# Kernel optimization log

Hardware: AMD Instinct MI355X
Metric: run time of the kernel (lower is better)

Reference implementation:

```python
import jax, jax.numpy as jnp
import numpy as np

O, D, E, K, H, A = 1024, 1024, 16, 4, 2048, 64  # option_dim, obs_dim, num_experts, k, moe_hidden, act_dim
LOSS_COEF = 0.01


def cv_squared(x):
    # torch .var() is unbiased (ddof=1)
    eps = 1e-10
    return jnp.var(x, ddof=1) / (jnp.mean(x) ** 2 + eps)


def setup_inputs() -> dict:
    key = jax.random.key(0)
    ks = jax.random.split(key, 8)
    s = 0.02
    return {
        "obs": jax.random.normal(ks[0], (O, D), jnp.float32),
        # original inits w_gate to zeros (degenerate top-k); use small random for a meaningful baseline
        "w_gate": jax.random.normal(ks[1], (O, D, E), jnp.float32) * s,
        "w1": jax.random.normal(ks[2], (E, D, H), jnp.float32) * s,   # expert MLP layer 1
        "b1": jnp.zeros((E, H), jnp.float32),
        "w2": jax.random.normal(ks[3], (E, H, A), jnp.float32) * s,   # expert MLP layer 2
        "b2": jnp.zeros((E, A), jnp.float32),
        "last_w": jax.random.normal(ks[4], (O, D, A), jnp.float32),   # last_w_layer
        "last_b": jax.random.normal(ks[5], (O, A), jnp.float32),      # last_b_layer
    }


def reference(obs, w_gate, w1, b1, w2, b2, last_w, last_b):
    # ---- noisy_top_k_gating (this version applies no noise) ----
    logits = jnp.einsum('od,ode->oe', obs, w_gate)                    # [O, E]
    top_vals, top_idx = jax.lax.top_k(logits, K + 1)
    topk_gates = jax.nn.softmax(top_vals[:, :K], axis=1)              # softmax over top-k logits
    rows = jnp.arange(O)[:, None]
    gates = jnp.zeros_like(logits).at[rows, top_idx[:, :K]].set(topk_gates)  # scatter -> [O, E]
    importance = gates.sum(axis=1)
    load = (gates > 0).sum(axis=1).astype(jnp.float32)                # faithful to original (sum over dim 1)
    loss = (cv_squared(importance) + cv_squared(load)) * LOSS_COEF
    # ---- dispatch / expert MLPs / combine (dense-over-experts equivalent; zero gates kill non-top-k) ----
    h = jax.nn.relu(jnp.einsum('od,edh->oeh', obs, w1) + b1[None])    # [O, E, H]
    y = jnp.einsum('oe,oeh,eha->oa', gates, h, w2) + gates @ b2       # [O, A]
    # ---- action head ----
    mu = jnp.einsum('od,oda->oa', obs, last_w) + last_b               # [O, A]
    action_probs = jax.nn.softmax(mu, axis=-1)
    z = (action_probs == 0.0).astype(action_probs.dtype) * 1e-08
    log_action_probs = jnp.log(action_probs + z)
    return (action_probs, log_action_probs, y, loss)
```

## Files before the change

### kernel.cpp

```cpp
#include <hip/hip_runtime.h>
#include <hip/hip_bf16.h>
#include <math.h>

#define O_ 1024
#define D_ 1024
#define E_ 16
#define K_ 4
#define H_ 2048
#define A_ 64
#define LOSS_COEF 0.01f

#define FLT_MIN_NORMAL 1.17549435e-38f

using floatx4 = __attribute__((ext_vector_type(4))) float;
using fragb   = __attribute__((ext_vector_type(8))) short;

static __device__ __forceinline__ ushort f2bf(float f) {
    unsigned u = __builtin_bit_cast(unsigned, f);
    u += 0x7fffu + ((u >> 16) & 1u);
    return (ushort)(u >> 16);
}

static __device__ __forceinline__ void gld_lds16(const void* g, void* l) {
    __builtin_amdgcn_global_load_lds(
        (const __attribute__((address_space(1))) void*)g,
        (__attribute__((address_space(3))) void*)l, 16, 0, 0);
}

__global__ __launch_bounds__(256) void front_kernel(
    const float* __restrict__ obs, const float* __restrict__ w_gate,
    const float* __restrict__ b2,
    const float* __restrict__ w1, const float* __restrict__ w2,
    int* __restrict__ cnt, int* __restrict__ rows, float* __restrict__ gatev,
    float* __restrict__ imp, float* __restrict__ loadv,
    ushort* __restrict__ obs_bf, float* __restrict__ yout,
    ushort* __restrict__ w1T, ushort* __restrict__ w2T)
{
    const int bid = blockIdx.x;
    const int t = threadIdx.x;
    __shared__ __align__(16) char sh[9344];

    if (bid < 1024) {
        const int o = bid;
        float* xs            = (float*)sh;
        float (*part)[20]    = (float(*)[20])(sh + 4096);
        float* logits        = (float*)(sh + 9216);
        int*   sidx          = (int*)(sh + 9280);
        float* sgate         = (float*)(sh + 9296);

        const float4* xrow = (const float4*)(obs + (size_t)o * D_);
        for (int i = t; i < D_ / 4; i += 256) ((float4*)xs)[i] = xrow[i];
        __syncthreads();

        const int dg = t >> 2, e4 = t & 3;
        const float4* wg = (const float4*)(w_gate + (size_t)o * (D_ * E_));
        float4 acc = make_float4(0.f, 0.f, 0.f, 0.f);
        #pragma unroll 4
        for (int i = 0; i < 16; ++i) {
            int d = dg + (i << 6);
            float4 w = wg[d * 4 + e4];
            float x = xs[d];
            acc.x += x * w.x; acc.y += x * w.y; acc.z += x * w.z; acc.w += x * w.w;
        }
        *(float4*)&part[dg][e4 * 4] = acc;
        __syncthreads();
        if (t < E_) {
            float s = 0.f;
            for (int g = 0; g < 64; ++g) s += part[g][t];
            logits[t] = s;
        }
        __syncthreads();
        if (t == 0) {
            float lv[E_];
            #pragma unroll
            for (int i = 0; i < E_; ++i) lv[i] = logits[i];
            int idx[K_]; float val[K_];
            bool used[E_] = {};
            for (int k = 0; k < K_; ++k) {
                int bi = 0; float bv = -INFINITY;
                for (int i = 0; i < E_; ++i)
                    if (!used[i] && lv[i] > bv) { bv = lv[i]; bi = i; }
                used[bi] = true; idx[k] = bi; val[k] = bv;
            }
            float m = val[0];
            float ex[K_]; float s = 0.f;
            for (int k = 0; k < K_; ++k) { ex[k] = expf(val[k] - m); s += ex[k]; }
            float inv = 1.f / s;
            float sumg = 0.f; int ld = 0;
            for (int k = 0; k < K_; ++k) {
                float g = ex[k] * inv;
                sidx[k] = idx[k]; sgate[k] = g;
                int pos = atomicAdd(&cnt[idx[k]], 1);
                rows[idx[k] * O_ + pos]  = o;
                gatev[idx[k] * O_ + pos] = g;
                sumg += g;
                if (g > 0.f) ld++;
            }
            imp[o] = sumg;
            loadv[o] = (float)ld;
        }

        {
            float4 v = ((const float4*)xs)[t];
            ushort4 u;
            u.x = f2bf(v.x); u.y = f2bf(v.y); u.z = f2bf(v.z); u.w = f2bf(v.w);
            ((ushort4*)(obs_bf + (size_t)o * D_))[t] = u;
        }
        __syncthreads();

        if (t < A_) {
            float accy = 0.f;
            #pragma unroll
            for (int k = 0; k < K_; ++k)
                accy += sgate[k] * b2[sidx[k] * A_ + t];
            yout[(size_t)o * A_ + t] = accy;
        }
        return;
    }

    {
        int id = bid - 1024;
        const float* src; ushort* dst; int R, C, c0, r0, e;
        if (id < 8192) {
            c0 = (id & 31) * 64; r0 = ((id >> 5) & 15) * 64; e = id >> 9;
            src = w1; dst = w1T; R = D_; C = H_;
        } else {
            id -= 8192;
            c0 = 0; r0 = (id & 31) * 64; e = id >> 5;
            src = w2; dst = w2T; R = H_; C = A_;
        }

        ushort (*tile)[72] = (ushort(*)[72])sh;
        const float* s = src + (size_t)e * R * C;
        const int rr = t >> 4, cq = t & 15;
        #pragma unroll
        for (int i = 0; i < 4; ++i) {
            int r = rr + i * 16;
            float4 v = *(const float4*)(s + (size_t)(r0 + r) * C + c0 + cq * 4);
            ushort4 u;
            u.x = f2bf(v.x); u.y = f2bf(v.y); u.z = f2bf(v.z); u.w = f2bf(v.w);
            *(ushort4*)&tile[r][cq * 4] = u;
        }
        __syncthreads();
        ushort* dbase = dst + (size_t)e * R * C;
        const int cc = t >> 4, rq = t & 15;
        #pragma unroll
        for (int i = 0; i < 4; ++i) {
            int c = cc + i * 16;
            ushort4 u;
            u.x = tile[rq * 4 + 0][c];
            u.y = tile[rq * 4 + 1][c];
            u.z = tile[rq * 4 + 2][c];
            u.w = tile[rq * 4 + 3][c];
            *(ushort4*)(dbase + (size_t)(c0 + c) * R + r0 + rq * 4) = u;
        }
    }
}

__global__ __launch_bounds__(256, 4) void mega_kernel(
    const ushort* __restrict__ obs_bf, const ushort* __restrict__ w1T,
    const float* __restrict__ b1, const ushort* __restrict__ w2T,
    const int* __restrict__ cnt, const int* __restrict__ rows,
    const float* __restrict__ gatev, float* __restrict__ y,
    const float* __restrict__ obs, const float* __restrict__ last_w,
    const float* __restrict__ last_b,
    float* __restrict__ probs, float* __restrict__ logprobs,
    const float* __restrict__ imp, const float* __restrict__ loadv,
    float* __restrict__ out_loss)
{
    const int bid = blockIdx.x;
    const int t = threadIdx.x;

    __shared__ __align__(16) ushort smem[17408];
    __shared__ int   rid_s[128];
    __shared__ float rgate_s[128];
    __shared__ float b1s[128];
    __shared__ float mean1, mean2;

    if (bid == 0) {
        float* ls1 = (float*)smem;
        float* ls2 = ls1 + 256;
        float a[4], b[4];
        float pa = 0.f, pb = 0.f;
        #pragma unroll
        for (int j = 0; j < 4; ++j) {
            a[j] = imp[t + 256 * j]; b[j] = loadv[t + 256 * j];
            pa += a[j]; pb += b[j];
        }
        ls1[t] = pa; ls2[t] = pb; __syncthreads();
        for (int s = 128; s > 0; s >>= 1) {
            if (t < s) { ls1[t] += ls1[t + s]; ls2[t] += ls2[t + s]; }
            __syncthreads();
        }
        if (t == 0) { mean1 = ls1[0] / O_; mean2 = ls2[0] / O_; }
        __syncthreads();
        pa = 0.f; pb = 0.f;
        #pragma unroll
        for (int j = 0; j < 4; ++j) {
            float d1 = a[j] - mean1, d2 = b[j] - mean2;
            pa += d1 * d1; pb += d2 * d2;
        }
        ls1[t] = pa; ls2[t] = pb; __syncthreads();
        for (int s = 128; s > 0; s >>= 1) {
            if (t < s) { ls1[t] += ls1[t + s]; ls2[t] += ls2[t + s]; }
            __syncthreads();
        }
        if (t == 0) {
            float var1 = ls1[0] / (O_ - 1), var2 = ls2[0] / (O_ - 1);
            const float eps = 1e-10f;
            out_loss[0] = (var1 / (mean1 * mean1 + eps) + var2 / (mean2 * mean2 + eps)) * LOSS_COEF;
        }
        return;
    }

    if (bid <= 2048) {
        const int id  = bid - 1;
        const int xcd = id & 7;
        const int r8  = (id >> 3) & 7;
        const int phi = id >> 6;
        const int p   = (phi << 3) | xcd;
        const int e   = p >> 4, ht = p & 15, rt = r8;
        const int n = cnt[e];
        if (rt * 128 >= n) return;

        const int wv = t >> 6, l = t & 63;
        const int lm = l & 15, q = l >> 4;
        const int wr = wv >> 1, wc = wv & 1;

        if (t < 128) {
            int gi = rt * 128 + t;
            rid_s[t]   = (gi < n) ? rows[e * O_ + gi]  : -1;
            rgate_s[t] = (gi < n) ? gatev[e * O_ + gi] : 0.f;
        } else {
            b1s[t - 128] = b1[e * H_ + ht * 128 + (t - 128)];
        }
        __syncthreads();

        const int swe = ((l & 7) ^ (l >> 3)) << 3;
        const ushort* asrc[4];
        const ushort* bsrc[4];
        #pragma unroll
        for (int j = 0; j < 4; ++j) {
            int r = (j * 4 + wv) * 8 + (l >> 3);
            int arow = rid_s[r]; if (arow < 0) arow = 0;
            asrc[j] = obs_bf + (size_t)arow * D_ + swe;
            bsrc[j] = w1T + ((size_t)(e * H_ + ht * 128 + r)) * D_ + swe;
        }

        auto stage = [&](int kc) {
            ushort* ab_ = &smem[0];
            ushort* bb_ = &smem[8192];
            const int ko = kc * 64;
            #pragma unroll
            for (int j = 0; j < 4; ++j) {
                gld_lds16(asrc[j] + ko, ab_ + (j * 4 + wv) * 512);
                gld_lds16(bsrc[j] + ko, bb_ + (j * 4 + wv) * 512);
            }
        };

        floatx4 acc[4][4] = {};
        const ushort* ab = &smem[0];
        const ushort* bb = &smem[8192];
        for (int kc = 0; kc < 16; ++kc) {
            stage(kc);
            __syncthreads();
            #pragma unroll
            for (int ks = 0; ks < 2; ++ks) {
                const int co = ((ks * 4 + q) ^ (lm & 7)) << 3;
                fragb a[4];
                #pragma unroll
                for (int i = 0; i < 4; ++i)
                    a[i] = *(const fragb*)(ab + (wr * 64 + i * 16 + lm) * 64 + co);
                #pragma unroll
                for (int nt = 0; nt < 4; ++nt) {
                    fragb b = *(const fragb*)(bb + (wc * 64 + nt * 16 + lm) * 64 + co);
                    #pragma unroll
                    for (int i = 0; i < 4; ++i)
                        acc[i][nt] = __builtin_amdgcn_mfma_f32_16x16x32_bf16(a[i], b, acc[i][nt], 0, 0, 0);
                }
            }
            __syncthreads();
        }

        ushort* Hs = smem;
        #pragma unroll
        for (int i = 0; i < 4; ++i) {
            #pragma unroll
            for (int nt = 0; nt < 4; ++nt) {
                const int col = wc * 64 + nt * 16 + lm;
                const float bb2 = b1s[col];
                #pragma unroll
                for (int r = 0; r < 4; ++r) {
                    const int row = wr * 64 + i * 16 + q * 4 + r;
                    float h = acc[i][nt][r] + bb2;
                    h = h > 0.f ? h : 0.f;
                    Hs[row * 136 + col] = f2bf(h * rgate_s[row]);
                }
            }
        }
        __syncthreads();

        floatx4 acc2[4][2] = {};
        #pragma unroll
        for (int ks = 0; ks < 4; ++ks) {
            fragb a[4];
            #pragma unroll
            for (int i = 0; i < 4; ++i)
                a[i] = *(const fragb*)(Hs + (wr * 64 + i * 16 + lm) * 136 + ks * 32 + q * 8);
            #pragma unroll
            for (int nt = 0; nt < 2; ++nt) {
                const int acol = wc * 32 + nt * 16 + lm;
                fragb b = *(const fragb*)(w2T + ((size_t)(e * A_ + acol)) * H_ + ht * 128 + ks * 32 + q * 8);
                #pragma unroll
                for (int i = 0; i < 4; ++i)
                    acc2[i][nt] = __builtin_amdgcn_mfma_f32_16x16x32_bf16(a[i], b, acc2[i][nt], 0, 0, 0);
            }
        }

        #pragma unroll
        for (int i = 0; i < 4; ++i) {
            #pragma unroll
            for (int r = 0; r < 4; ++r) {
                const int row = wr * 64 + i * 16 + q * 4 + r;
                const int orow = rid_s[row];
                if (orow >= 0) {
                    #pragma unroll
                    for (int nt = 0; nt < 2; ++nt)
                        atomicAdd(&y[(size_t)orow * A_ + wc * 32 + nt * 16 + lm], acc2[i][nt][r]);
                }
            }
        }
        return;
    }

    {
        const int o = bid - 2049;
        float* xs = (float*)smem;
        float (*red)[A_] = (float(*)[A_])(smem + 2048);

        const float4* xrow = (const float4*)(obs + (size_t)o * D_);
        for (int i = t; i < D_ / 4; i += 256) ((float4*)xs)[i] = xrow[i];
        __syncthreads();

        const int a4 = t & 15, dg = t >> 4;
        const float* lw = last_w + (size_t)o * (D_ * A_);
        float acc0 = 0.f, acc1 = 0.f, acc2 = 0.f, acc3 = 0.f;
        #pragma unroll 8
        for (int i = 0; i < D_ / 16; ++i) {
            int d = dg + (i << 4);
            float4 w = *(const float4*)(lw + (size_t)d * A_ + a4 * 4);
            float x = xs[d];
            acc0 += x * w.x; acc1 += x * w.y; acc2 += x * w.z; acc3 += x * w.w;
        }
        *(float4*)&red[dg][a4 * 4] = make_float4(acc0, acc1, acc2, acc3);
        __syncthreads();

        if (t < A_) {
            float mu = last_b[(size_t)o * A_ + t];
            #pragma unroll
            for (int g = 0; g < 16; ++g) mu += red[g][t];
            float mx = mu;
            #pragma unroll
            for (int off = 32; off > 0; off >>= 1) mx = fmaxf(mx, __shfl_xor(mx, off, 64));
            float ex = expf(mu - mx);
            if (ex < FLT_MIN_NORMAL) ex = 0.f;
            float s = ex;
            #pragma unroll
            for (int off = 32; off > 0; off >>= 1) s += __shfl_xor(s, off, 64);
            float p = ex / s;
            if (p < FLT_MIN_NORMAL) p = 0.f;
            probs[(size_t)o * A_ + t] = p;
            float z = (p == 0.f) ? 1e-8f : 0.f;
            logprobs[(size_t)o * A_ + t] = logf(p + z);
        }
    }
}

extern "C" void kernel_launch(void* const* d_in, const int* in_sizes, int n_in,
                              void* d_out, int out_size, void* d_ws, size_t ws_size,
                              hipStream_t stream)
{
    const float* obs    = (const float*)d_in[0];
    const float* w_gate = (const float*)d_in[1];
    const float* w1     = (const float*)d_in[2];
    const float* b1     = (const float*)d_in[3];
    const float* w2     = (const float*)d_in[4];
    const float* b2     = (const float*)d_in[5];
    const float* last_w = (const float*)d_in[6];
    const float* last_b = (const float*)d_in[7];

    float* out   = (float*)d_out;
    float* probs = out;
    float* logp  = out + O_ * A_;
    float* yout  = out + 2 * O_ * A_;
    float* loss  = out + 3 * O_ * A_;

    char* ws = (char*)d_ws;
    float*  imp       = (float*)(ws + (32 << 10));
    float*  loadv     = (float*)(ws + (36 << 10));
    int*    cnt       = (int*)(ws + (40 << 10));
    int*    rows      = (int*)(ws + (41 << 10));
    float*  gatev     = (float*)(ws + (105 << 10));
    ushort* obs_bf    = (ushort*)(ws + (256 << 10));
    ushort* w1T       = (ushort*)(ws + (256 << 10) + (2 << 20));
    ushort* w2T       = (ushort*)(ws + (256 << 10) + (66 << 20));

    hipMemsetAsync(cnt, 0, E_ * sizeof(int), stream);

    hipLaunchKernelGGL(front_kernel, dim3(1024 + 8192 + 512), dim3(256), 0, stream,
                       obs, w_gate, b2, w1, w2,
                       cnt, rows, gatev, imp, loadv, obs_bf, yout, w1T, w2T);
    hipLaunchKernelGGL(mega_kernel, dim3(1 + 2048 + 1024), dim3(256), 0, stream,
                       obs_bf, w1T, b1, w2T, cnt, rows, gatev, yout,
                       obs, last_w, last_b, probs, logp, imp, loadv, loss);
}
```

Before: 553.1 us.

## Split mega kernel and double-buffer LDS staging in expert GEMM

Splits the combined mega kernel into a dedicated expert GEMM kernel and a separate action-head/loss kernel, launched one after the other. The expert kernel now double-buffers its LDS tiles, issuing the next K-chunk's global-to-LDS loads while computing on the current one, which removes one barrier per iteration. This doubles LDS use and lowers the occupancy hint from 4 to 2 blocks per CU. It also adds an extra launch, and the bandwidth-bound action head no longer runs alongside the expert blocks.

```diff
diff --git a/kernel.cpp b/kernel.cpp
--- a/kernel.cpp
+++ b/kernel.cpp
@@ -157,11 +157,140 @@
     }
 }
 
-__global__ __launch_bounds__(256, 4) void mega_kernel(
+__global__ __launch_bounds__(256, 2) void expert_kernel(
     const ushort* __restrict__ obs_bf, const ushort* __restrict__ w1T,
     const float* __restrict__ b1, const ushort* __restrict__ w2T,
     const int* __restrict__ cnt, const int* __restrict__ rows,
-    const float* __restrict__ gatev, float* __restrict__ y,
+    const float* __restrict__ gatev, float* __restrict__ y)
+{
+    const int id  = blockIdx.x;
+    const int xcd = id & 7;
+    const int r8  = (id >> 3) & 7;
+    const int phi = id >> 6;
+    const int p   = (phi << 3) | xcd;
+    const int e   = p >> 4, ht = p & 15, rt = r8;
+    const int n = cnt[e];
+    if (rt * 128 >= n) return;
+
+    const int t = threadIdx.x, wv = t >> 6, l = t & 63;
+    const int lm = l & 15, q = l >> 4;
+    const int wr = wv >> 1, wc = wv & 1;
+
+    __shared__ __align__(16) ushort smem[32768];
+    __shared__ int   rid_s[128];
+    __shared__ float rgate_s[128];
+    __shared__ float b1s[128];
+
+    if (t < 128) {
+        int gi = rt * 128 + t;
+        rid_s[t]   = (gi < n) ? rows[e * O_ + gi]  : -1;
+        rgate_s[t] = (gi < n) ? gatev[e * O_ + gi] : 0.f;
+    } else {
+        b1s[t - 128] = b1[e * H_ + ht * 128 + (t - 128)];
+    }
+    __syncthreads();
+
+    const int swe = ((l & 7) ^ (l >> 3)) << 3;
+    const ushort* asrc[4];
+    const ushort* bsrc[4];
+    #pragma unroll
+    for (int j = 0; j < 4; ++j) {
+        int r = (j * 4 + wv) * 8 + (l >> 3);
+        int arow = rid_s[r]; if (arow < 0) arow = 0;
+        asrc[j] = obs_bf + (size_t)arow * D_ + swe;
+        bsrc[j] = w1T + ((size_t)(e * H_ + ht * 128 + r)) * D_ + swe;
+    }
+
+    auto stage = [&](int b, int kc) {
+        ushort* ab_ = &smem[b * 8192];
+        ushort* bb_ = &smem[16384 + b * 8192];
+        const int ko = kc * 64;
+        #pragma unroll
+        for (int j = 0; j < 4; ++j) {
+            gld_lds16(asrc[j] + ko, ab_ + (j * 4 + wv) * 512);
+            gld_lds16(bsrc[j] + ko, bb_ + (j * 4 + wv) * 512);
+        }
+    };
+
+    floatx4 acc[4][4] = {};
+    int buf = 0;
+    stage(0, 0);
+    __syncthreads();
+
+    for (int kc = 0; kc < 16; ++kc) {
+        if (kc < 15) stage(buf ^ 1, kc + 1);
+        const ushort* ab = &smem[buf * 8192];
+        const ushort* bb = &smem[16384 + buf * 8192];
+        #pragma unroll
+        for (int ks = 0; ks < 2; ++ks) {
+            const int co = ((ks * 4 + q) ^ (lm & 7)) << 3;
+            fragb a[4];
+            #pragma unroll
+            for (int i = 0; i < 4; ++i)
+                a[i] = *(const fragb*)(ab + (wr * 64 + i * 16 + lm) * 64 + co);
+            #pragma unroll
+            for (int nt = 0; nt < 4; ++nt) {
+                fragb b = *(const fragb*)(bb + (wc * 64 + nt * 16 + lm) * 64 + co);
+                #pragma unroll
+                for (int i = 0; i < 4; ++i)
+                    acc[i][nt] = __builtin_amdgcn_mfma_f32_16x16x32_bf16(a[i], b, acc[i][nt], 0, 0, 0);
+            }
+        }
+        __syncthreads();
+        buf ^= 1;
+    }
+
+    ushort* Hs = smem;
+    #pragma unroll
+    for (int i = 0; i < 4; ++i) {
+        #pragma unroll
+        for (int nt = 0; nt < 4; ++nt) {
+            const int col = wc * 64 + nt * 16 + lm;
+            const float bb2 = b1s[col];
+            #pragma unroll
+            for (int r = 0; r < 4; ++r) {
+                const int row = wr * 64 + i * 16 + q * 4 + r;
+                float h = acc[i][nt][r] + bb2;
+                h = h > 0.f ? h : 0.f;
+                Hs[row * 136 + col] = f2bf(h * rgate_s[row]);
+            }
+        }
+    }
+    __syncthreads();
+
+    floatx4 acc2[4][2] = {};
+    #pragma unroll
+    for (int ks = 0; ks < 4; ++ks) {
+        fragb a[4];
+        #pragma unroll
+        for (int i = 0; i < 4; ++i)
+            a[i] = *(const fragb*)(Hs + (wr * 64 + i * 16 + lm) * 136 + ks * 32 + q * 8);
+        #pragma unroll
+        for (int nt = 0; nt < 2; ++nt) {
+            const int acol = wc * 32 + nt * 16 + lm;
+            fragb b = *(const fragb*)(w2T + ((size_t)(e * A_ + acol)) * H_ + ht * 128 + ks * 32 + q * 8);
+            #pragma unroll
+            for (int i = 0; i < 4; ++i)
+                acc2[i][nt] = __builtin_amdgcn_mfma_f32_16x16x32_bf16(a[i], b, acc2[i][nt], 0, 0, 0);
+        }
+    }
+
+    #pragma unroll
+    for (int i = 0; i < 4; ++i) {
+        #pragma unroll
+        for (int r = 0; r < 4; ++r) {
+            const int row = wr * 64 + i * 16 + q * 4 + r;
+            const int orow = rid_s[row];
+            if (orow >= 0) {
+                #pragma unroll
+                for (int nt = 0; nt < 2; ++nt)
+                    atomicAdd(&y[(size_t)orow * A_ + wc * 32 + nt * 16 + lm], acc2[i][nt][r]);
+            }
+        }
+    }
+}
+
+__global__ __launch_bounds__(256) void action_loss_kernel(
     const float* __restrict__ obs, const float* __restrict__ last_w,
     const float* __restrict__ last_b,
     float* __restrict__ probs, float* __restrict__ logprobs,
@@ -171,15 +300,12 @@
     const int bid = blockIdx.x;
     const int t = threadIdx.x;
 
-    __shared__ __align__(16) ushort smem[17408];
-    __shared__ int   rid_s[128];
-    __shared__ float rgate_s[128];
-    __shared__ float b1s[128];
+    __shared__ float xs[D_];
+    __shared__ float red[16][A_];
+    __shared__ float ls1[256], ls2[256];
     __shared__ float mean1, mean2;
 
-    if (bid == 0) {
-        float* ls1 = (float*)smem;
-        float* ls2 = ls1 + 256;
+    if (bid == 1024) {
         float a[4], b[4];
         float pa = 0.f, pb = 0.f;
         #pragma unroll
@@ -213,166 +339,42 @@
         return;
     }
 
-    if (bid <= 2048) {
-        const int id  = bid - 1;
-        const int xcd = id & 7;
-        const int r8  = (id >> 3) & 7;
-        const int phi = id >> 6;
-        const int p   = (phi << 3) | xcd;
-        const int e   = p >> 4, ht = p & 15, rt = r8;
-        const int n = cnt[e];
-        if (rt * 128 >= n) return;
-
-        const int wv = t >> 6, l = t & 63;
-        const int lm = l & 15, q = l >> 4;
-        const int wr = wv >> 1, wc = wv & 1;
-
-        if (t < 128) {
-            int gi = rt * 128 + t;
-            rid_s[t]   = (gi < n) ? rows[e * O_ + gi]  : -1;
-            rgate_s[t] = (gi < n) ? gatev[e * O_ + gi] : 0.f;
-        } else {
-            b1s[t - 128] = b1[e * H_ + ht * 128 + (t - 128)];
-        }
-        __syncthreads();
-
-        const int swe = ((l & 7) ^ (l >> 3)) << 3;
-        const ushort* asrc[4];
-        const ushort* bsrc[4];
-        #pragma unroll
-        for (int j = 0; j < 4; ++j) {
-            int r = (j * 4 + wv) * 8 + (l >> 3);
-            int arow = rid_s[r]; if (arow < 0) arow = 0;
-            asrc[j] = obs_bf + (size_t)arow * D_ + swe;
-            bsrc[j] = w1T + ((size_t)(e * H_ + ht * 128 + r)) * D_ + swe;
-        }
-
-        auto stage = [&](int kc) {
-            ushort* ab_ = &smem[0];
-            ushort* bb_ = &smem[8192];
-            const int ko = kc * 64;
-            #pragma unroll
-            for (int j = 0; j < 4; ++j) {
-                gld_lds16(asrc[j] + ko, ab_ + (j * 4 + wv) * 512);
-                gld_lds16(bsrc[j] + ko, bb_ + (j * 4 + wv) * 512);
-            }
-        };
-
-        floatx4 acc[4][4] = {};
-        const ushort* ab = &smem[0];
-        const ushort* bb = &smem[8192];
-        for (int kc = 0; kc < 16; ++kc) {
-            stage(kc);
-            __syncthreads();
-            #pragma unroll
-            for (int ks = 0; ks < 2; ++ks) {
-                const int co = ((ks * 4 + q) ^ (lm & 7)) << 3;
-                fragb a[4];
-                #pragma unroll
-                for (int i = 0; i < 4; ++i)
-                    a[i] = *(const fragb*)(ab + (wr * 64 + i * 16 + lm) * 64 + co);
-                #pragma unroll
-                for (int nt = 0; nt < 4; ++nt) {
-                    fragb b = *(const fragb*)(bb + (wc * 64 + nt * 16 + lm) * 64 + co);
-                    #pragma unroll
-                    for (int i = 0; i < 4; ++i)
-                        acc[i][nt] = __builtin_amdgcn_mfma_f32_16x16x32_bf16(a[i], b, acc[i][nt], 0, 0, 0);
-                }
-            }
-            __syncthreads();
-        }
-
-        ushort* Hs = smem;
-        #pragma unroll
-        for (int i = 0; i < 4; ++i) {
-            #pragma unroll
-            for (int nt = 0; nt < 4; ++nt) {
-                const int col = wc * 64 + nt * 16 + lm;
-                const float bb2 = b1s[col];
-                #pragma unroll
-                for (int r = 0; r < 4; ++r) {
-                    const int row = wr * 64 + i * 16 + q * 4 + r;
-                    float h = acc[i][nt][r] + bb2;
-                    h = h > 0.f ? h : 0.f;
-                    Hs[row * 136 + col] = f2bf(h * rgate_s[row]);
-                }
-            }
-        }
-        __syncthreads();
-
-        floatx4 acc2[4][2] = {};
-        #pragma unroll
-        for (int ks = 0; ks < 4; ++ks) {
-            fragb a[4];
-            #pragma unroll
-            for (int i = 0; i < 4; ++i)
-                a[i] = *(const fragb*)(Hs + (wr * 64 + i * 16 + lm) * 136 + ks * 32 + q * 8);
-            #pragma unroll
-            for (int nt = 0; nt < 2; ++nt) {
-                const int acol = wc * 32 + nt * 16 + lm;
-                fragb b = *(const fragb*)(w2T + ((size_t)(e * A_ + acol)) * H_ + ht * 128 + ks * 32 + q * 8);
-                #pragma unroll
-                for (int i = 0; i < 4; ++i)
-                    acc2[i][nt] = __builtin_amdgcn_mfma_f32_16x16x32_bf16(a[i], b, acc2[i][nt], 0, 0, 0);
-            }
-        }
-
-        #pragma unroll
-        for (int i = 0; i < 4; ++i) {
-            #pragma unroll
-            for (int r = 0; r < 4; ++r) {
-                const int row = wr * 64 + i * 16 + q * 4 + r;
-                const int orow = rid_s[row];
-                if (orow >= 0) {
-                    #pragma unroll
-                    for (int nt = 0; nt < 2; ++nt)
-                        atomicAdd(&y[(size_t)orow * A_ + wc * 32 + nt * 16 + lm], acc2[i][nt][r]);
-                }
-            }
-        }
-        return;
-    }
-
-    {
-        const int o = bid - 2049;
-        float* xs = (float*)smem;
-        float (*red)[A_] = (float(*)[A_])(smem + 2048);
-
-        const float4* xrow = (const float4*)(obs + (size_t)o * D_);
-        for (int i = t; i < D_ / 4; i += 256) ((float4*)xs)[i] = xrow[i];
-        __syncthreads();
-
-        const int a4 = t & 15, dg = t >> 4;
-        const float* lw = last_w + (size_t)o * (D_ * A_);
-        float acc0 = 0.f, acc1 = 0.f, acc2 = 0.f, acc3 = 0.f;
-        #pragma unroll 8
-        for (int i = 0; i < D_ / 16; ++i) {
-            int d = dg + (i << 4);
-            float4 w = *(const float4*)(lw + (size_t)d * A_ + a4 * 4);
-            float x = xs[d];
-            acc0 += x * w.x; acc1 += x * w.y; acc2 += x * w.z; acc3 += x * w.w;
-        }
-        *(float4*)&red[dg][a4 * 4] = make_float4(acc0, acc1, acc2, acc3);
-        __syncthreads();
-
-        if (t < A_) {
-            float mu = last_b[(size_t)o * A_ + t];
-            #pragma unroll
-            for (int g = 0; g < 16; ++g) mu += red[g][t];
-            float mx = mu;
-            #pragma unroll
-            for (int off = 32; off > 0; off >>= 1) mx = fmaxf(mx, __shfl_xor(mx, off, 64));
-            float ex = expf(mu - mx);
-            if (ex < FLT_MIN_NORMAL) ex = 0.f;
-            float s = ex;
-            #pragma unroll
-            for (int off = 32; off > 0; off >>= 1) s += __shfl_xor(s, off, 64);
-            float p = ex / s;
-            if (p < FLT_MIN_NORMAL) p = 0.f;
-            probs[(size_t)o * A_ + t] = p;
-            float z = (p == 0.f) ? 1e-8f : 0.f;
-            logprobs[(size_t)o * A_ + t] = logf(p + z);
-        }
+    const int o = bid;
+
+    const float4* xrow = (const float4*)(obs + (size_t)o * D_);
+    for (int i = t; i < D_ / 4; i += 256) ((float4*)xs)[i] = xrow[i];
+    __syncthreads();
+
+    const int a4 = t & 15, dg = t >> 4;
+    const float* lw = last_w + (size_t)o * (D_ * A_);
+    float acc0 = 0.f, acc1 = 0.f, acc2 = 0.f, acc3 = 0.f;
+    #pragma unroll 8
+    for (int i = 0; i < D_ / 16; ++i) {
+        int d = dg + (i << 4);
+        float4 w = *(const float4*)(lw + (size_t)d * A_ + a4 * 4);
+        float x = xs[d];
+        acc0 += x * w.x; acc1 += x * w.y; acc2 += x * w.z; acc3 += x * w.w;
+    }
+    *(float4*)&red[dg][a4 * 4] = make_float4(acc0, acc1, acc2, acc3);
+    __syncthreads();
+
+    if (t < A_) {
+        float mu = last_b[(size_t)o * A_ + t];
+        #pragma unroll
+        for (int g = 0; g < 16; ++g) mu += red[g][t];
+        float mx = mu;
+        #pragma unroll
+        for (int off = 32; off > 0; off >>= 1) mx = fmaxf(mx, __shfl_xor(mx, off, 64));
+        float ex = expf(mu - mx);
+        if (ex < FLT_MIN_NORMAL) ex = 0.f;
+        float s = ex;
+        #pragma unroll
+        for (int off = 32; off > 0; off >>= 1) s += __shfl_xor(s, off, 64);
+        float p = ex / s;
+        if (p < FLT_MIN_NORMAL) p = 0.f;
+        probs[(size_t)o * A_ + t] = p;
+        float z = (p == 0.f) ? 1e-8f : 0.f;
+        logprobs[(size_t)o * A_ + t] = logf(p + z);
     }
 }
 
@@ -410,7 +412,8 @@
     hipLaunchKernelGGL(front_kernel, dim3(1024 + 8192 + 512), dim3(256), 0, stream,
                        obs, w_gate, b2, w1, w2,
                        cnt, rows, gatev, imp, loadv, obs_bf, yout, w1T, w2T);
-    hipLaunchKernelGGL(mega_kernel, dim3(1 + 2048 + 1024), dim3(256), 0, stream,
-                       obs_bf, w1T, b1, w2T, cnt, rows, gatev, yout,
+    hipLaunchKernelGGL(expert_kernel, dim3(2048), dim3(256), 0, stream,
+                       obs_bf, w1T, b1, w2T, cnt, rows, gatev, yout);
+    hipLaunchKernelGGL(action_loss_kernel, dim3(1025), dim3(256), 0, stream,
                        obs, last_w, last_b, probs, logp, imp, loadv, loss);
 }
```

New measurement: 565.9 us. 2.3% more time.
